# Optimization experiments

Measured on AMD Instinct MI355X. Metric: run time of the kernel, lower is better.

## Reference

```python
import jax, jax.numpy as jnp
import numpy as np

F_DIM = 128
N_RBF = 20
CUTOFF = 5.0
N_LAYERS = 3
EPS = 1e-8


def setup_inputs() -> dict:
    key = jax.random.key(0)
    ks = jax.random.split(key, 16)
    N, E = 10000, 320000
    atomic_numbers = jax.random.randint(ks[0], (N,), 0, 100)
    r_ij = jax.random.normal(ks[1], (E, 3), dtype=jnp.float32)
    idx_i = jnp.sort(jax.random.randint(ks[2], (E,), 0, N))
    idx_j = jax.random.randint(ks[3], (E,), 0, N)
    emb = jax.random.normal(ks[4], (100, F_DIM), dtype=jnp.float32)
    emb = emb.at[0].set(0.0)  # padding_idx=0
    s = 0.05
    return {
        "atomic_numbers": atomic_numbers,
        "r_ij": r_ij,
        "idx_i": idx_i,
        "idx_j": idx_j,
        "embedding": emb,
        "filt_W": jax.random.normal(ks[5], (N_RBF, N_LAYERS * 3 * F_DIM), dtype=jnp.float32) * s,
        "filt_b": jax.random.normal(ks[6], (N_LAYERS * 3 * F_DIM,), dtype=jnp.float32) * s,
        "int_W1": jax.random.normal(ks[7], (N_LAYERS, F_DIM, F_DIM), dtype=jnp.float32) * s,
        "int_b1": jax.random.normal(ks[8], (N_LAYERS, F_DIM), dtype=jnp.float32) * s,
        "int_W2": jax.random.normal(ks[9], (N_LAYERS, F_DIM, 3 * F_DIM), dtype=jnp.float32) * s,
        "int_b2": jax.random.normal(ks[10], (N_LAYERS, 3 * F_DIM), dtype=jnp.float32) * s,
        "mix_W1": jax.random.normal(ks[11], (N_LAYERS, 2 * F_DIM, F_DIM), dtype=jnp.float32) * s,
        "mix_b1": jax.random.normal(ks[12], (N_LAYERS, F_DIM), dtype=jnp.float32) * s,
        "mix_W2": jax.random.normal(ks[13], (N_LAYERS, F_DIM, 3 * F_DIM), dtype=jnp.float32) * s,
        "mix_b2": jax.random.normal(ks[14], (N_LAYERS, 3 * F_DIM), dtype=jnp.float32) * s,
        "mux_W": jax.random.normal(ks[15], (N_LAYERS, F_DIM, 2 * F_DIM), dtype=jnp.float32) * s,
    }


def _painn(embedding, filt_W, filt_b, int_W1, int_b1, int_W2, int_b2,
           mix_W1, mix_b1, mix_W2, mix_b2, mux_W,
           r_ij, atomic_numbers, idx_i, idx_j):
    N = atomic_numbers.shape[0]
    F = F_DIM
    d_ij = jnp.linalg.norm(r_ij, axis=1, keepdims=True)          # [E,1]
    dir_ij = r_ij / d_ij                                          # [E,3]
    # Gaussian RBF expansion
    offset = jnp.linspace(0.0, CUTOFF, N_RBF, dtype=jnp.float32)
    coeff = -0.5 / (offset[1] - offset[0]) ** 2
    phi = jnp.exp(coeff * (d_ij[..., None] - offset) ** 2)        # [E,1,n_rbf]
    # Cosine cutoff
    fcut = 0.5 * (jnp.cos(d_ij * jnp.pi / CUTOFF) + 1.0) * (d_ij < CUTOFF)  # [E,1]
    filters = (phi @ filt_W + filt_b) * fcut[..., None]           # [E,1,L*3F]
    filter_list = jnp.split(filters, N_LAYERS, axis=-1)

    q = embedding[atomic_numbers][:, None, :]                     # [N,1,F]
    mu = jnp.zeros((N, 3, F), dtype=q.dtype)

    for i in range(N_LAYERS):
        Wij = filter_list[i]                                      # [E,1,3F]
        # interaction
        h = jax.nn.silu(q @ int_W1[i] + int_b1[i])
        x = h @ int_W2[i] + int_b2[i]                             # [N,1,3F]
        xj = x[idx_j]                                             # [E,1,3F]
        muj = mu[idx_j]                                           # [E,3,F]
        xw = Wij * xj
        dq, dmuR, dmumu = jnp.split(xw, 3, axis=-1)               # each [E,1,F]
        dq = jax.ops.segment_sum(dq, idx_i, num_segments=N)       # [N,1,F]
        dmu = dmuR * dir_ij[:, :, None] + dmumu * muj             # [E,3,F]
        dmu = jax.ops.segment_sum(dmu, idx_i, num_segments=N)     # [N,3,F]
        q = q + dq
        mu = mu + dmu
        # mixing
        mu_mix = mu @ mux_W[i]                                    # [N,3,2F]
        mu_V, mu_W = jnp.split(mu_mix, 2, axis=-1)
        mu_Vn = jnp.sqrt(jnp.sum(mu_V ** 2, axis=-2, keepdims=True) + EPS)  # [N,1,F]
        ctx = jnp.concatenate([q, mu_Vn], axis=-1)                # [N,1,2F]
        h = jax.nn.silu(ctx @ mix_W1[i] + mix_b1[i])
        x = h @ mix_W2[i] + mix_b2[i]                             # [N,1,3F]
        dq_i, dmu_i, dqmu_i = jnp.split(x, 3, axis=-1)
        dmu_i = dmu_i * mu_W                                      # [N,3,F]
        dqmu_i = dqmu_i * jnp.sum(mu_V * mu_W, axis=1, keepdims=True)
        q = q + dq_i + dqmu_i
        mu = mu + dmu_i
    return q[:, 0, :], mu


def reference(atomic_numbers, r_ij, idx_i, idx_j, embedding, filt_W, filt_b,
              int_W1, int_b1, int_W2, int_b2, mix_W1, mix_b1, mix_W2, mix_b2, mux_W):
    return _painn(embedding, filt_W, filt_b, int_W1, int_b1, int_W2, int_b2,
                  mix_W1, mix_b1, mix_W2, mix_b2, mux_W,
                  r_ij, atomic_numbers, idx_i, idx_j)
```

## Files before the change

kernel.cpp:

```cpp
#include <hip/hip_runtime.h>
#include <hip/hip_bf16.h>

#define F_DIM 128
#define N_RBF 20
#define CUTOFF 5.0f
#define PI_F 3.14159265358979323846f
#define NPB 4

typedef float v2f __attribute__((ext_vector_type(2)));
typedef __attribute__((ext_vector_type(8))) short bf16x8;
typedef __attribute__((ext_vector_type(4))) float f32x4;

__device__ __forceinline__ unsigned int bf16_rtne(float f) {
    unsigned int u = __float_as_uint(f);
    u += 0x7fffu + ((u >> 16) & 1u);
    return u >> 16;
}
__device__ __forceinline__ unsigned int pack_bf2(float lo, float hi) {
    return bf16_rtne(lo) | (bf16_rtne(hi) << 16);
}
__device__ __forceinline__ float unpk_lo(unsigned int u) {
    return __uint_as_float(u << 16);
}
__device__ __forceinline__ float unpk_hi(unsigned int u) {
    return __uint_as_float(u & 0xffff0000u);
}
__device__ __forceinline__ float bf16_to_f(unsigned short s) {
    return __uint_as_float(((unsigned int)s) << 16);
}

__global__ __launch_bounds__(256) void k_rowptr(const int* __restrict__ idx_i,
                                                int* __restrict__ row_ptr, int N, int E) {
    int i = blockIdx.x * blockDim.x + threadIdx.x;
    if (i > N) return;
    if (i == N) { row_ptr[N] = E; return; }
    int lo = 0, hi = E;
    while (lo < hi) {
        int mid = (lo + hi) >> 1;
        if (idx_i[mid] < i) lo = mid + 1; else hi = mid;
    }
    row_ptr[i] = lo;
}

__global__ __launch_bounds__(256) void k_init(const int* __restrict__ Z,
                                              const float* __restrict__ emb,
                                              float* __restrict__ q,
                                              unsigned int* __restrict__ P,
                                              float* __restrict__ muD, int N) {
    int idx = blockIdx.x * blockDim.x + threadIdx.x;
    if (idx < N * F_DIM) {
        int n = idx >> 7, f = idx & 127;
        q[idx] = emb[Z[n] * F_DIM + f];
    }
    if (idx < N * 384) { P[idx] = 0u; muD[idx] = 0.f; }
}

__global__ __launch_bounds__(256) void k_prep(const float* __restrict__ muxW,
                                              const float* __restrict__ W1,
                                              const float* __restrict__ W2,
                                              const float* __restrict__ iW1,
                                              const float* __restrict__ iW2,
                                              unsigned short* __restrict__ muxWt,
                                              unsigned short* __restrict__ W1t,
                                              unsigned short* __restrict__ W2t,
                                              unsigned short* __restrict__ iW1t,
                                              unsigned short* __restrict__ iW2t) {
    int idx = blockIdx.x * 256 + threadIdx.x;
    if (idx < 98304) {
        int l = idx / 32768, rem = idx % 32768;
        int c = rem / 128, k = rem % 128;
        muxWt[idx] = (unsigned short)bf16_rtne(muxW[l * 32768 + k * 256 + c]);
    } else if (idx < 196608) {
        int i2 = idx - 98304;
        int l = i2 / 32768, rem = i2 % 32768;
        int c = rem / 256, k = rem % 256;
        W1t[i2] = (unsigned short)bf16_rtne(W1[l * 32768 + k * 128 + c]);
    } else if (idx < 344064) {
        int i2 = idx - 196608;
        int l = i2 / 49152, rem = i2 % 49152;
        int c = rem / 128, k = rem % 128;
        W2t[i2] = (unsigned short)bf16_rtne(W2[l * 49152 + k * 384 + c]);
    } else if (idx < 393216) {
        int i2 = idx - 344064;
        int l = i2 / 16384, rem = i2 % 16384;
        int c = rem / 128, k = rem % 128;
        iW1t[i2] = (unsigned short)bf16_rtne(iW1[l * 16384 + k * 128 + c]);
    } else if (idx < 540672) {
        int i2 = idx - 393216;
        int l = i2 / 49152, rem = i2 % 49152;
        int c = rem / 128, k = rem % 128;
        iW2t[i2] = (unsigned short)bf16_rtne(iW2[l * 49152 + k * 384 + c]);
    }
}

__global__ __launch_bounds__(256) void k_geom(const float* __restrict__ r,
                                              float* __restrict__ geom, int E) {
    int e = blockIdx.x * blockDim.x + threadIdx.x;
    if (e >= E) return;
    float x = r[e * 3], y = r[e * 3 + 1], z = r[e * 3 + 2];
    float d = sqrtf(x * x + y * y + z * z);
    float inv = 1.f / d;
    float fc = (d < CUTOFF) ? 0.5f * (__cosf(d * (PI_F / CUTOFF)) + 1.f) : 0.f;
    float* g = geom + (size_t)e * 24;
    g[0] = x * inv; g[1] = y * inv; g[2] = z * inv; g[3] = fc;
    const float delta = CUTOFF / (N_RBF - 1);
    const float coeff = -0.5f / (delta * delta);
#pragma unroll
    for (int k = 0; k < N_RBF; k++) {
        float t = d - k * delta;
        g[4 + k] = __expf(coeff * t * t) * fc;
    }
}

__global__ __launch_bounds__(256) void k_node_mfma(
        const float* __restrict__ q,
        const unsigned short* __restrict__ iW1t,
        const float* __restrict__ b1,
        const unsigned short* __restrict__ iW2t,
        const float* __restrict__ b2,
        unsigned int* __restrict__ P, int N) {
    __shared__ unsigned short A[16 * 136];
    __shared__ unsigned short Ah[16 * 136];
    __shared__ float Xs[16 * 396];
    int t = threadIdx.x;
    int w = t >> 6, l = t & 63, quad = l >> 4, c0 = l & 15;
    int n0 = blockIdx.x * 16;

#pragma unroll
    for (int i = 0; i < 4; i++) {
        int flat = i * 256 + t;
        int node = flat >> 6, cp = flat & 63;
        int gn = n0 + node;
        unsigned int v = 0u;
        if (gn < N) { const float* s = q + (size_t)gn * 128 + 2 * cp; v = pack_bf2(s[0], s[1]); }
        *(unsigned int*)&A[node * 136 + 2 * cp] = v;
    }
    __syncthreads();

    bf16x8 a1[4];
#pragma unroll
    for (int ks = 0; ks < 4; ks++)
        a1[ks] = *(const bf16x8*)&A[c0 * 136 + ks * 32 + quad * 8];
#pragma unroll
    for (int jj = 0; jj < 2; jj++) {
        int jg = 2 * w + jj;
        float bb = b1[16 * jg + c0];
        f32x4 acc = (f32x4){bb, bb, bb, bb};
#pragma unroll
        for (int ks = 0; ks < 4; ks++) {
            bf16x8 b = *(const bf16x8*)&iW1t[(16 * jg + c0) * 128 + ks * 32 + quad * 8];
            acc = __builtin_amdgcn_mfma_f32_16x16x32_bf16(a1[ks], b, acc, 0, 0, 0);
        }
#pragma unroll
        for (int r = 0; r < 4; r++) {
            float aa = acc[r];
            Ah[(quad * 4 + r) * 136 + 16 * jg + c0] =
                (unsigned short)bf16_rtne(aa / (1.f + __expf(-aa)));
        }
    }
    __syncthreads();

    bf16x8 a3[4];
#pragma unroll
    for (int ks = 0; ks < 4; ks++)
        a3[ks] = *(const bf16x8*)&Ah[c0 * 136 + ks * 32 + quad * 8];
#pragma unroll
    for (int jj = 0; jj < 6; jj++) {
        int jx = 6 * w + jj;
        float bb = b2[16 * jx + c0];
        f32x4 acc = (f32x4){bb, bb, bb, bb};
#pragma unroll
        for (int ks = 0; ks < 4; ks++) {
            bf16x8 b = *(const bf16x8*)&iW2t[(16 * jx + c0) * 128 + ks * 32 + quad * 8];
            acc = __builtin_amdgcn_mfma_f32_16x16x32_bf16(a3[ks], b, acc, 0, 0, 0);
        }
#pragma unroll
        for (int r = 0; r < 4; r++)
            Xs[(quad * 4 + r) * 396 + 16 * jx + c0] = acc[r];
    }
    __syncthreads();

    int n = t >> 4, fi = (t & 15) * 8;
    int gn = n0 + n;
    if (gn < N) {
        size_t base = (size_t)gn * 384;
        unsigned int d[8];
#pragma unroll
        for (int k = 0; k < 8; k++) {
            float x0 = Xs[n * 396 + fi + k];
            float x1 = Xs[n * 396 + 128 + fi + k];
            float x2 = Xs[n * 396 + 256 + fi + k];
            d[k] = pack_bf2(x0, x1);
            ((unsigned short*)&P[base + 256 + fi + k])[0] = (unsigned short)bf16_rtne(x2);
        }
        *(uint4*)&P[base + fi]     = make_uint4(d[0], d[1], d[2], d[3]);
        *(uint4*)&P[base + fi + 4] = make_uint4(d[4], d[5], d[6], d[7]);
    }
}

__global__ __launch_bounds__(256) void k_edge(const unsigned int* __restrict__ P,
                                              const float* __restrict__ geom,
                                              const int* __restrict__ idx_j,
                                              const int* __restrict__ row_ptr,
                                              const float* __restrict__ filt_W,
                                              const float* __restrict__ filt_b,
                                              int layer,
                                              float* __restrict__ q,
                                              float* __restrict__ muD, int N) {
    __shared__ float red[4][128];
    int t = threadIdx.x;
    int f = t & 127;
    int sub = __builtin_amdgcn_readfirstlane(t >> 7);

    v2f W0p[N_RBF / 2], W1p[N_RBF / 2], W2p[N_RBF / 2];
    const float* Wbase = filt_W + layer * 384;
#pragma unroll
    for (int j = 0; j < N_RBF / 2; j++) {
        W0p[j] = (v2f){Wbase[(2 * j) * 1152 + f],       Wbase[(2 * j + 1) * 1152 + f]};
        W1p[j] = (v2f){Wbase[(2 * j) * 1152 + 128 + f], Wbase[(2 * j + 1) * 1152 + 128 + f]};
        W2p[j] = (v2f){Wbase[(2 * j) * 1152 + 256 + f], Wbase[(2 * j + 1) * 1152 + 256 + f]};
    }
    float bf0 = filt_b[layer * 384 + f];
    float bf1 = filt_b[layer * 384 + 128 + f];
    float bf2 = filt_b[layer * 384 + 256 + f];

    int i0 = blockIdx.x * NPB;
    for (int nn = 0; nn < NPB; nn++) {
        int i = i0 + nn;
        if (i >= N) break;
        int rs = __builtin_amdgcn_readfirstlane(row_ptr[i]);
        int re = __builtin_amdgcn_readfirstlane(row_ptr[i + 1]);
        float dq = 0.f;
        v2f dm01 = (v2f){0.f, 0.f};
        float dm2 = 0.f;

        for (int e = rs + sub; e < re; e += 2) {
            int j = __builtin_amdgcn_readfirstlane(idx_j[e]);
            const unsigned int* Pj = P + (size_t)j * 384;
            unsigned int A = Pj[f];
            unsigned int B = Pj[128 + f];
            unsigned int C = Pj[256 + f];

            const float4* g4 = (const float4*)(geom + (size_t)e * 24);
            float4 a  = g4[0];
            float4 p0 = g4[1], p1 = g4[2], p2 = g4[3], p3 = g4[4], p4 = g4[5];

            v2f ph[N_RBF / 2] = {
                (v2f){p0.x, p0.y}, (v2f){p0.z, p0.w},
                (v2f){p1.x, p1.y}, (v2f){p1.z, p1.w},
                (v2f){p2.x, p2.y}, (v2f){p2.z, p2.w},
                (v2f){p3.x, p3.y}, (v2f){p3.z, p3.w},
                (v2f){p4.x, p4.y}, (v2f){p4.z, p4.w}};
            v2f aq = (v2f){0.f, 0.f}, ar = (v2f){0.f, 0.f}, am = (v2f){0.f, 0.f};
#pragma unroll
            for (int k = 0; k < N_RBF / 2; k++) {
                aq += ph[k] * W0p[k];
                ar += ph[k] * W1p[k];
                am += ph[k] * W2p[k];
            }
            float wq = aq.x + aq.y + a.w * bf0;
            float wr = ar.x + ar.y + a.w * bf1;
            float wm = am.x + am.y + a.w * bf2;

            float xq = unpk_lo(A), xr = unpk_hi(A);
            float m0 = unpk_lo(B), m1 = unpk_hi(B);
            float xm = unpk_lo(C), m2 = unpk_hi(C);

            dq += wq * xq;
            float s_r = wr * xr, s_m = wm * xm;
            dm01 += (v2f){s_r, s_r} * (v2f){a.x, a.y} + (v2f){s_m, s_m} * (v2f){m0, m1};
            dm2  += s_r * a.z + s_m * m2;
        }

        if (sub == 1) { red[0][f] = dq; red[1][f] = dm01.x; red[2][f] = dm01.y; red[3][f] = dm2; }
        __syncthreads();
        if (sub == 0) {
            dq += red[0][f];
            float d0 = dm01.x + red[1][f], d1 = dm01.y + red[2][f];
            dm2 += red[3][f];
            q[(size_t)i * 128 + f] += dq;
            size_t base = (size_t)i * 384;
            muD[base + f]       += d0;
            muD[base + 128 + f] += d1;
            muD[base + 256 + f] += dm2;
        }
        __syncthreads();
    }
}

__global__ __launch_bounds__(256) void k_mix_mfma(
        float* __restrict__ q, float* __restrict__ mu,
        const unsigned short* __restrict__ muxWt,
        const unsigned short* __restrict__ W1t,
        const unsigned short* __restrict__ W2t,
        const float* __restrict__ b1,
        const float* __restrict__ b2,
        unsigned int* __restrict__ P, int N) {
    __shared__ unsigned short A[16 * 264];
    __shared__ unsigned short Ah[16 * 136];
    __shared__ unsigned short Wsp[3 * 16 * 136];
    __shared__ float Xs[16 * 396];
    __shared__ float Ss[16 * 140];
    int t = threadIdx.x;
    int w = t >> 6, l = t & 63, quad = l >> 4, c0 = l & 15;
    int n0 = blockIdx.x * 16;

#pragma unroll
    for (int i = 0; i < 4; i++) {
        int flat = i * 256 + t;
        int node = flat >> 6, cp = flat & 63;
        int gn = n0 + node;
        unsigned int v = 0u;
        if (gn < N) { const float* s = q + (size_t)gn * 128 + 2 * cp; v = pack_bf2(s[0], s[1]); }
        *(unsigned int*)&A[node * 264 + 2 * cp] = v;
    }

    f32x4 vn2[2], S[2];
#pragma unroll
    for (int jj = 0; jj < 2; jj++) { vn2[jj] = (f32x4){0,0,0,0}; S[jj] = (f32x4){0,0,0,0}; }

    for (int c = 0; c < 3; c++) {
#pragma unroll
        for (int i = 0; i < 4; i++) {
            int flat = i * 256 + t;
            int node = flat >> 6, cp = flat & 63;
            int gn = n0 + node;
            unsigned int v = 0u;
            if (gn < N) {
                const float* s = mu + (size_t)gn * 384 + c * 128 + 2 * cp;
                v = pack_bf2(s[0], s[1]);
            }
            *(unsigned int*)&A[node * 264 + 128 + 2 * cp] = v;
        }
        __syncthreads();
        bf16x8 af[4];
#pragma unroll
        for (int ks = 0; ks < 4; ks++)
            af[ks] = *(const bf16x8*)&A[c0 * 264 + 128 + ks * 32 + quad * 8];
#pragma unroll
        for (int jj = 0; jj < 2; jj++) {
            int jv = 2 * w + jj;
            f32x4 V = (f32x4){0,0,0,0}, Wm = (f32x4){0,0,0,0};
#pragma unroll
            for (int ks = 0; ks < 4; ks++) {
                bf16x8 bV = *(const bf16x8*)&muxWt[(16 * jv + c0) * 128 + ks * 32 + quad * 8];
                V = __builtin_amdgcn_mfma_f32_16x16x32_bf16(af[ks], bV, V, 0, 0, 0);
            }
#pragma unroll
            for (int ks = 0; ks < 4; ks++) {
                bf16x8 bW = *(const bf16x8*)&muxWt[(16 * (jv + 8) + c0) * 128 + ks * 32 + quad * 8];
                Wm = __builtin_amdgcn_mfma_f32_16x16x32_bf16(af[ks], bW, Wm, 0, 0, 0);
            }
            vn2[jj] += V * V;
            S[jj]   += V * Wm;
#pragma unroll
            for (int r = 0; r < 4; r++)
                Wsp[c * 2176 + (quad * 4 + r) * 136 + 16 * jv + c0] =
                    (unsigned short)bf16_rtne(Wm[r]);
        }
        __syncthreads();
    }

#pragma unroll
    for (int jj = 0; jj < 2; jj++) {
        int jv = 2 * w + jj;
#pragma unroll
        for (int r = 0; r < 4; r++)
            A[(quad * 4 + r) * 264 + 128 + 16 * jv + c0] =
                (unsigned short)bf16_rtne(sqrtf(vn2[jj][r] + 1e-8f));
    }
    __syncthreads();

    bf16x8 a2[8];
#pragma unroll
    for (int ks = 0; ks < 8; ks++)
        a2[ks] = *(const bf16x8*)&A[c0 * 264 + ks * 32 + quad * 8];
#pragma unroll
    for (int jj = 0; jj < 2; jj++) {
        int jg = 2 * w + jj;
        float bb = b1[16 * jg + c0];
        f32x4 acc = (f32x4){bb, bb, bb, bb};
#pragma unroll
        for (int ks = 0; ks < 8; ks++) {
            bf16x8 b = *(const bf16x8*)&W1t[(16 * jg + c0) * 256 + ks * 32 + quad * 8];
            acc = __builtin_amdgcn_mfma_f32_16x16x32_bf16(a2[ks], b, acc, 0, 0, 0);
        }
#pragma unroll
        for (int r = 0; r < 4; r++) {
            float aa = acc[r];
            Ah[(quad * 4 + r) * 136 + 16 * jg + c0] =
                (unsigned short)bf16_rtne(aa / (1.f + __expf(-aa)));
        }
    }
    __syncthreads();

    bf16x8 a3[4];
#pragma unroll
    for (int ks = 0; ks < 4; ks++)
        a3[ks] = *(const bf16x8*)&Ah[c0 * 136 + ks * 32 + quad * 8];
#pragma unroll
    for (int jj = 0; jj < 6; jj++) {
        int jx = 6 * w + jj;
        float bb = b2[16 * jx + c0];
        f32x4 acc = (f32x4){bb, bb, bb, bb};
#pragma unroll
        for (int ks = 0; ks < 4; ks++) {
            bf16x8 b = *(const bf16x8*)&W2t[(16 * jx + c0) * 128 + ks * 32 + quad * 8];
            acc = __builtin_amdgcn_mfma_f32_16x16x32_bf16(a3[ks], b, acc, 0, 0, 0);
        }
#pragma unroll
        for (int r = 0; r < 4; r++)
            Xs[(quad * 4 + r) * 396 + 16 * jx + c0] = acc[r];
    }
#pragma unroll
    for (int jj = 0; jj < 2; jj++) {
        int jv = 2 * w + jj;
#pragma unroll
        for (int r = 0; r < 4; r++)
            Ss[(quad * 4 + r) * 140 + 16 * jv + c0] = S[jj][r];
    }
    __syncthreads();

    int n = t >> 4, fi = (t & 15) * 8;
    int gn = n0 + n;
    if (gn < N) {
        float* qp = q + (size_t)gn * 128 + fi;
#pragma unroll
        for (int k = 0; k < 8; k++)
            qp[k] = qp[k] + Xs[n * 396 + fi + k] +
                    Xs[n * 396 + 256 + fi + k] * Ss[n * 140 + fi + k];
        size_t base = (size_t)gn * 384;
        float m[3][8];
#pragma unroll
        for (int c = 0; c < 3; c++) {
            float* mp = mu + base + c * 128 + fi;
#pragma unroll
            for (int k = 0; k < 8; k++) {
                m[c][k] = mp[k] + Xs[n * 396 + 128 + fi + k] *
                                  bf16_to_f(Wsp[c * 2176 + n * 136 + fi + k]);
                mp[k] = m[c][k];
            }
        }
        unsigned int d[8];
#pragma unroll
        for (int k = 0; k < 8; k++) {
            d[k] = pack_bf2(m[0][k], m[1][k]);
            ((unsigned short*)&P[base + 256 + fi + k])[1] = (unsigned short)bf16_rtne(m[2][k]);
        }
        *(uint4*)&P[base + 128 + fi]     = make_uint4(d[0], d[1], d[2], d[3]);
        *(uint4*)&P[base + 128 + fi + 4] = make_uint4(d[4], d[5], d[6], d[7]);
    }
}

extern "C" void kernel_launch(void* const* d_in, const int* in_sizes, int n_in,
                              void* d_out, int out_size, void* d_ws, size_t ws_size,
                              hipStream_t stream) {
    const int*   Z      = (const int*)d_in[0];
    const float* r_ij   = (const float*)d_in[1];
    const int*   idx_i  = (const int*)d_in[2];
    const int*   idx_j  = (const int*)d_in[3];
    const float* emb    = (const float*)d_in[4];
    const float* filt_W = (const float*)d_in[5];
    const float* filt_b = (const float*)d_in[6];
    const float* int_W1 = (const float*)d_in[7];
    const float* int_b1 = (const float*)d_in[8];
    const float* int_W2 = (const float*)d_in[9];
    const float* int_b2 = (const float*)d_in[10];
    const float* mix_W1 = (const float*)d_in[11];
    const float* mix_b1 = (const float*)d_in[12];
    const float* mix_W2 = (const float*)d_in[13];
    const float* mix_b2 = (const float*)d_in[14];
    const float* mux_W  = (const float*)d_in[15];

    int N = in_sizes[0];
    int E = in_sizes[2];

    float* q   = (float*)d_out;
    float* muD = q + (size_t)N * 128;

    float* ws   = (float*)d_ws;
    float* geom = ws;
    unsigned int* P = (unsigned int*)(geom + (size_t)E * 24);
    int* row_ptr = (int*)(P + (size_t)N * 384);
    uintptr_t waddr = (uintptr_t)(row_ptr + N + 1);
    waddr = (waddr + 15) & ~(uintptr_t)15;
    unsigned short* muxWt = (unsigned short*)waddr;
    unsigned short* W1t   = muxWt + 98304;
    unsigned short* W2t   = W1t + 98304;
    unsigned short* iW1t  = W2t + 147456;
    unsigned short* iW2t  = iW1t + 49152;

    k_rowptr<<<(N + 1 + 255) / 256, 256, 0, stream>>>(idx_i, row_ptr, N, E);
    k_init<<<((size_t)N * 384 + 255) / 256, 256, 0, stream>>>(Z, emb, q, P, muD, N);
    k_geom<<<(E + 255) / 256, 256, 0, stream>>>(r_ij, geom, E);
    k_prep<<<2112, 256, 0, stream>>>(mux_W, mix_W1, mix_W2, int_W1, int_W2,
                                     muxWt, W1t, W2t, iW1t, iW2t);

    int tiles = (N + 15) / 16;
    for (int l = 0; l < 3; l++) {
        k_node_mfma<<<tiles, 256, 0, stream>>>(
            q, iW1t + (size_t)l * 16384, int_b1 + l * 128,
            iW2t + (size_t)l * 49152, int_b2 + l * 384, P, N);
        k_edge<<<(N + NPB - 1) / NPB, 256, 0, stream>>>(
            P, geom, idx_j, row_ptr, filt_W, filt_b, l, q, muD, N);
        k_mix_mfma<<<tiles, 256, 0, stream>>>(
            q, muD, muxWt + (size_t)l * 32768, W1t + (size_t)l * 32768,
            W2t + (size_t)l * 49152, mix_b1 + l * 128, mix_b2 + l * 384, P, N);
    }
}
```

Baseline: 599.5 us.

## Fuse next layer's node MLP into mixing kernel epilogue

The per-layer node-interaction MLP (q -> W1 -> silu -> W2, written as packed bf16 into P) is now computed at the end of the mixing kernel for the next layer, reusing the freshly updated q held in shared memory. This removes two separate kernel launches and the global re-read of q between mixing and the next layer's node stage. Only the first layer's node kernel stays standalone. It adds shared-memory reuse (Ah aliased onto Wsp and into A) and extra barriers, and k_edge gets a launch-bounds occupancy hint of 4 blocks.

```diff
diff --git a/kernel.cpp b/kernel.cpp
--- a/kernel.cpp
+++ b/kernel.cpp
@@ -198,15 +198,16 @@
     }
 }
 
-__global__ __launch_bounds__(256) void k_edge(const unsigned int* __restrict__ P,
-                                              const float* __restrict__ geom,
-                                              const int* __restrict__ idx_j,
-                                              const int* __restrict__ row_ptr,
-                                              const float* __restrict__ filt_W,
-                                              const float* __restrict__ filt_b,
-                                              int layer,
-                                              float* __restrict__ q,
-                                              float* __restrict__ muD, int N) {
+__global__ __launch_bounds__(256, 4) void k_edge(
+        const unsigned int* __restrict__ P,
+        const float* __restrict__ geom,
+        const int* __restrict__ idx_j,
+        const int* __restrict__ row_ptr,
+        const float* __restrict__ filt_W,
+        const float* __restrict__ filt_b,
+        int layer,
+        float* __restrict__ q,
+        float* __restrict__ muD, int N) {
     __shared__ float red[4][128];
     int t = threadIdx.x;
     int f = t & 127;
@@ -288,16 +289,20 @@
     }
 }
 
-__global__ __launch_bounds__(256) void k_mix_mfma(
+__global__ __launch_bounds__(256) void k_mix_fused(
         float* __restrict__ q, float* __restrict__ mu,
         const unsigned short* __restrict__ muxWt,
         const unsigned short* __restrict__ W1t,
         const unsigned short* __restrict__ W2t,
         const float* __restrict__ b1,
         const float* __restrict__ b2,
+        const unsigned short* __restrict__ niW1t,
+        const float* __restrict__ nib1,
+        const unsigned short* __restrict__ niW2t,
+        const float* __restrict__ nib2,
+        int has_node,
         unsigned int* __restrict__ P, int N) {
     __shared__ unsigned short A[16 * 264];
-    __shared__ unsigned short Ah[16 * 136];
     __shared__ unsigned short Wsp[3 * 16 * 136];
     __shared__ float Xs[16 * 396];
     __shared__ float Ss[16 * 140];
@@ -375,21 +380,31 @@
 #pragma unroll
     for (int ks = 0; ks < 8; ks++)
         a2[ks] = *(const bf16x8*)&A[c0 * 264 + ks * 32 + quad * 8];
-#pragma unroll
-    for (int jj = 0; jj < 2; jj++) {
-        int jg = 2 * w + jj;
-        float bb = b1[16 * jg + c0];
-        f32x4 acc = (f32x4){bb, bb, bb, bb};
-#pragma unroll
-        for (int ks = 0; ks < 8; ks++) {
-            bf16x8 b = *(const bf16x8*)&W1t[(16 * jg + c0) * 256 + ks * 32 + quad * 8];
-            acc = __builtin_amdgcn_mfma_f32_16x16x32_bf16(a2[ks], b, acc, 0, 0, 0);
-        }
-#pragma unroll
-        for (int r = 0; r < 4; r++) {
-            float aa = acc[r];
-            Ah[(quad * 4 + r) * 136 + 16 * jg + c0] =
-                (unsigned short)bf16_rtne(aa / (1.f + __expf(-aa)));
+    {
+        unsigned short htmp[2][4];
+#pragma unroll
+        for (int jj = 0; jj < 2; jj++) {
+            int jg = 2 * w + jj;
+            float bb = b1[16 * jg + c0];
+            f32x4 acc = (f32x4){bb, bb, bb, bb};
+#pragma unroll
+            for (int ks = 0; ks < 8; ks++) {
+                bf16x8 b = *(const bf16x8*)&W1t[(16 * jg + c0) * 256 + ks * 32 + quad * 8];
+                acc = __builtin_amdgcn_mfma_f32_16x16x32_bf16(a2[ks], b, acc, 0, 0, 0);
+            }
+#pragma unroll
+            for (int r = 0; r < 4; r++) {
+                float aa = acc[r];
+                htmp[jj][r] = (unsigned short)bf16_rtne(aa / (1.f + __expf(-aa)));
+            }
+        }
+        __syncthreads();
+#pragma unroll
+        for (int jj = 0; jj < 2; jj++) {
+            int jg = 2 * w + jj;
+#pragma unroll
+            for (int r = 0; r < 4; r++)
+                A[(quad * 4 + r) * 264 + 128 + 16 * jg + c0] = htmp[jj][r];
         }
     }
     __syncthreads();
@@ -397,7 +412,7 @@
     bf16x8 a3[4];
 #pragma unroll
     for (int ks = 0; ks < 4; ks++)
-        a3[ks] = *(const bf16x8*)&Ah[c0 * 136 + ks * 32 + quad * 8];
+        a3[ks] = *(const bf16x8*)&A[c0 * 264 + 128 + ks * 32 + quad * 8];
 #pragma unroll
     for (int jj = 0; jj < 6; jj++) {
         int jx = 6 * w + jj;
@@ -425,10 +440,18 @@
     int gn = n0 + n;
     if (gn < N) {
         float* qp = q + (size_t)gn * 128 + fi;
-#pragma unroll
-        for (int k = 0; k < 8; k++)
-            qp[k] = qp[k] + Xs[n * 396 + fi + k] +
+        float qn[8];
+#pragma unroll
+        for (int k = 0; k < 8; k++) {
+            qn[k] = qp[k] + Xs[n * 396 + fi + k] +
                     Xs[n * 396 + 256 + fi + k] * Ss[n * 140 + fi + k];
+            qp[k] = qn[k];
+        }
+        unsigned int qd[4];
+#pragma unroll
+        for (int p = 0; p < 4; p++) qd[p] = pack_bf2(qn[2 * p], qn[2 * p + 1]);
+        *(uint4*)&A[n * 264 + fi] = make_uint4(qd[0], qd[1], qd[2], qd[3]);
+
         size_t base = (size_t)gn * 384;
         float m[3][8];
 #pragma unroll
@@ -449,6 +472,68 @@
         }
         *(uint4*)&P[base + 128 + fi]     = make_uint4(d[0], d[1], d[2], d[3]);
         *(uint4*)&P[base + 128 + fi + 4] = make_uint4(d[4], d[5], d[6], d[7]);
+    }
+    __syncthreads();
+
+    if (has_node) {
+        unsigned short* Ah = Wsp;
+        bf16x8 a1[4];
+#pragma unroll
+        for (int ks = 0; ks < 4; ks++)
+            a1[ks] = *(const bf16x8*)&A[c0 * 264 + ks * 32 + quad * 8];
+#pragma unroll
+        for (int jj = 0; jj < 2; jj++) {
+            int jg = 2 * w + jj;
+            float bb = nib1[16 * jg + c0];
+            f32x4 acc = (f32x4){bb, bb, bb, bb};
+#pragma unroll
+            for (int ks = 0; ks < 4; ks++) {
+                bf16x8 b = *(const bf16x8*)&niW1t[(16 * jg + c0) * 128 + ks * 32 + quad * 8];
+                acc = __builtin_amdgcn_mfma_f32_16x16x32_bf16(a1[ks], b, acc, 0, 0, 0);
+            }
+#pragma unroll
+            for (int r = 0; r < 4; r++) {
+                float aa = acc[r];
+                Ah[(quad * 4 + r) * 136 + 16 * jg + c0] =
+                    (unsigned short)bf16_rtne(aa / (1.f + __expf(-aa)));
+            }
+        }
+        __syncthreads();
+
+        bf16x8 a4[4];
+#pragma unroll
+        for (int ks = 0; ks < 4; ks++)
+            a4[ks] = *(const bf16x8*)&Ah[c0 * 136 + ks * 32 + quad * 8];
+#pragma unroll
+        for (int jj = 0; jj < 6; jj++) {
+            int jx = 6 * w + jj;
+            float bb = nib2[16 * jx + c0];
+            f32x4 acc = (f32x4){bb, bb, bb, bb};
+#pragma unroll
+            for (int ks = 0; ks < 4; ks++) {
+                bf16x8 b = *(const bf16x8*)&niW2t[(16 * jx + c0) * 128 + ks * 32 + quad * 8];
+                acc = __builtin_amdgcn_mfma_f32_16x16x32_bf16(a4[ks], b, acc, 0, 0, 0);
+            }
+#pragma unroll
+            for (int r = 0; r < 4; r++)
+                Xs[(quad * 4 + r) * 396 + 16 * jx + c0] = acc[r];
+        }
+        __syncthreads();
+
+        if (gn < N) {
+            size_t base = (size_t)gn * 384;
+            unsigned int d[8];
+#pragma unroll
+            for (int k = 0; k < 8; k++) {
+                float x0 = Xs[n * 396 + fi + k];
+                float x1 = Xs[n * 396 + 128 + fi + k];
+                float x2 = Xs[n * 396 + 256 + fi + k];
+                d[k] = pack_bf2(x0, x1);
+                ((unsigned short*)&P[base + 256 + fi + k])[0] = (unsigned short)bf16_rtne(x2);
+            }
+            *(uint4*)&P[base + fi]     = make_uint4(d[0], d[1], d[2], d[3]);
+            *(uint4*)&P[base + fi + 4] = make_uint4(d[4], d[5], d[6], d[7]);
+        }
     }
 }
 
@@ -497,14 +582,17 @@
                                      muxWt, W1t, W2t, iW1t, iW2t);
 
     int tiles = (N + 15) / 16;
+    k_node_mfma<<<tiles, 256, 0, stream>>>(
+        q, iW1t, int_b1, iW2t, int_b2, P, N);
     for (int l = 0; l < 3; l++) {
-        k_node_mfma<<<tiles, 256, 0, stream>>>(
-            q, iW1t + (size_t)l * 16384, int_b1 + l * 128,
-            iW2t + (size_t)l * 49152, int_b2 + l * 384, P, N);
         k_edge<<<(N + NPB - 1) / NPB, 256, 0, stream>>>(
             P, geom, idx_j, row_ptr, filt_W, filt_b, l, q, muD, N);
-        k_mix_mfma<<<tiles, 256, 0, stream>>>(
+        int nl = (l < 2) ? (l + 1) : 0;
+        k_mix_fused<<<tiles, 256, 0, stream>>>(
             q, muD, muxWt + (size_t)l * 32768, W1t + (size_t)l * 32768,
-            W2t + (size_t)l * 49152, mix_b1 + l * 128, mix_b2 + l * 384, P, N);
-    }
-}
+            W2t + (size_t)l * 49152, mix_b1 + l * 128, mix_b2 + l * 384,
+            iW1t + (size_t)nl * 16384, int_b1 + nl * 128,
+            iW2t + (size_t)nl * 49152, int_b2 + nl * 384,
+            (l < 2) ? 1 : 0, P, N);
+    }
+}
```

After: 585.4 us. -2.4%, faster.
